# Kernel optimization log

Measured on AMD Instinct MI355X. Metric: run time of the kernel, lower is better.

The kernel has to match this reference:

```python
import jax, jax.numpy as jnp
import numpy as np

N_NODES = 2708      # hardcoded in GCN.__init__ (DictLearn(2708, nfeat/2))
NFEAT = 4096
M_DICT = NFEAT // 2 # dictionary atoms
NHID = 1024
NCLASS = 64
POWER_ITER = 100
FISTA_ITER = 20


def power_method(W, key):
    # nm -> largest eigenvalue of W^T W (sigma_max(W)^2)
    X0 = jax.random.normal(key, (1, W.shape[1]), dtype=W.dtype)
    def body(i, carry):
        X, _ = carry
        Xn = (X @ W.T) @ W
        nm = jnp.linalg.norm(Xn)
        return (Xn / nm, nm)
    _, nm = jax.lax.fori_loop(0, POWER_ITER, body, (X0, jnp.float32(1.0)))
    return nm


def soft_threshold(X, lam):
    return jnp.sign(X) * jax.nn.relu(jnp.abs(X) - lam)


def fista(Y, W, lam, key):
    # torch sets W.requires_grad_(False) during sparse coding
    Ws = jax.lax.stop_gradient(W)
    c = power_method(Ws, key)
    eta = 1.0 / c
    Gamma0 = soft_threshold((eta * Ws).T @ Y, lam)   # (m, nfeat)
    Ynorm = jnp.linalg.norm(Y)
    def step(carry, _):
        Gamma, Z, t = carry
        residual = Ws @ Z - Y                         # (n, nfeat)
        Gamma_new = soft_threshold(Z - eta * (Ws.T @ residual), lam / c)
        t_new = (1.0 + jnp.sqrt(1.0 + 4.0 * t * t)) / 2.0
        Z_new = Gamma_new + (t - 1.0) / t_new * (Gamma_new - Gamma)
        nrm = jnp.linalg.norm(residual) / Ynorm
        return (Gamma_new, Z_new, t_new), nrm
    (Gamma, _, _), norms = jax.lax.scan(
        step, (Gamma0, Gamma0, jnp.float32(1.0)), None, length=FISTA_ITER)
    return Gamma, norms


def setup_inputs() -> dict:
    key = jax.random.key(0)
    ks = jax.random.split(key, 7)
    x = jax.random.normal(ks[0], (N_NODES, NFEAT), dtype=jnp.float32)
    # dense stand-in for the normalized sparse adjacency; scaled to keep activations sane
    adj = jax.random.uniform(ks[1], (N_NODES, N_NODES), dtype=jnp.float32) / N_NODES
    stdv1 = 1.0 / np.sqrt(NHID)
    gc1_w = jax.random.uniform(ks[2], (NFEAT, NHID), minval=-stdv1, maxval=stdv1, dtype=jnp.float32)
    gc1_b = jax.random.uniform(ks[3], (NHID,), minval=-stdv1, maxval=stdv1, dtype=jnp.float32)
    stdv2 = 1.0 / np.sqrt(NCLASS)
    gc2_w = jax.random.uniform(ks[4], (NHID, NCLASS), minval=-stdv2, maxval=stdv2, dtype=jnp.float32)
    gc2_b = jax.random.uniform(ks[5], (NCLASS,), minval=-stdv2, maxval=stdv2, dtype=jnp.float32)
    # torch normalizes W in-place via .data, so the learnable leaf IS the normalized dict
    W_dict = jax.random.normal(ks[6], (N_NODES, M_DICT), dtype=jnp.float32)
    W_dict = W_dict / jnp.linalg.norm(W_dict, axis=0, keepdims=True)
    return {"x": x, "adj": adj, "gc1_w": gc1_w, "gc1_b": gc1_b,
            "gc2_w": gc2_w, "gc2_b": gc2_b, "W_dict": W_dict, "K": 1}


def reference(x, adj, gc1_w, gc1_b, gc2_w, gc2_b, W_dict, K):
    # SC='fista' (the only dimensionally consistent path); K acts as lamda
    lam = jnp.float32(K)
    Gamma, norms = fista(x, W_dict, lam, jax.random.key(1))  # (m, nfeat)
    x_dec = W_dict @ Gamma                                   # (n, nfeat)
    h = jax.nn.relu(adj @ (x_dec @ gc1_w) + gc1_b)           # dropout is identity in eval
    out = adj @ (h @ gc2_w) + gc2_b
    return jax.nn.log_softmax(out, axis=1), x_dec, Gamma, norms
```

## Files before the change

### kernel.cpp

```cpp
#include <hip/hip_runtime.h>
#include <cstdint>
#include <cmath>

#define NN_ 2708
#define NF_ 4096
#define MD_ 2048
#define NH_ 1024
#define NC_ 64
#define FITER 20
#define KPAD 2720


typedef _Float16 half8_t __attribute__((ext_vector_type(8)));
typedef _Float16 half4_t __attribute__((ext_vector_type(4)));
typedef float floatx4_t __attribute__((ext_vector_type(4)));

__device__ __forceinline__ float softt(float v, float t) {
    float a = fabsf(v) - t;
    a = a > 0.f ? a : 0.f;
    return copysignf(a, v);
}

__device__ __forceinline__ float blockReduceSum(float v, float* red) {
    int lane = threadIdx.x & 63, wid = threadIdx.x >> 6;
    #pragma unroll
    for (int off = 32; off; off >>= 1) v += __shfl_down(v, off);
    if (lane == 0) red[wid] = v;
    __syncthreads();
    if (wid == 0) {
        int nw = (blockDim.x + 63) >> 6;
        float r = (lane < nw) ? red[lane] : 0.f;
        #pragma unroll
        for (int off = 4; off; off >>= 1) r += __shfl_down(r, off);
        if (lane == 0) red[0] = r;
    }
    __syncthreads();
    float out = red[0];
    __syncthreads();
    return out;
}

__device__ __forceinline__ float erfinv_f(float x) {
    float w = -log1pf(-x * x);
    float p;
    if (w < 5.0f) {
        w -= 2.5f;
        p = 2.81022636e-08f;
        p = fmaf(p, w, 3.43273939e-07f);
        p = fmaf(p, w, -3.5233877e-06f);
        p = fmaf(p, w, -4.39150654e-06f);
        p = fmaf(p, w, 0.00021858087f);
        p = fmaf(p, w, -0.00125372503f);
        p = fmaf(p, w, -0.00417768164f);
        p = fmaf(p, w, 0.246640727f);
        p = fmaf(p, w, 1.50140941f);
    } else {
        w = sqrtf(w) - 3.0f;
        p = -0.000200214257f;
        p = fmaf(p, w, 0.000100950558f);
        p = fmaf(p, w, 0.00134934322f);
        p = fmaf(p, w, -0.00367342844f);
        p = fmaf(p, w, 0.00573950773f);
        p = fmaf(p, w, -0.0076224613f);
        p = fmaf(p, w, 0.00943887047f);
        p = fmaf(p, w, 1.00167406f);
        p = fmaf(p, w, 2.83297682f);
    }
    return p * x;
}

__device__ __forceinline__ float u32_to_normal(uint32_t bits) {
    uint32_t fb = (bits >> 9) | 0x3F800000u;
    float f = __uint_as_float(fb) - 1.0f;
    const float lo = -0.99999994f;
    float u = fmaf(f, 2.0f, lo);
    u = fmaxf(lo, u);
    return 1.41421356f * erfinv_f(u);
}

__global__ void init_x0_kernel(float* __restrict__ X0) {
    int i = blockIdx.x * blockDim.x + threadIdx.x;
    if (i >= MD_ / 2) return;
    uint32_t x0 = (uint32_t)i, x1 = (uint32_t)(i + MD_ / 2);
    const uint32_t k0 = 0u, k1 = 1u, k2 = 0x1BD11BDBu;
    const uint32_t ks[3] = {k0, k1, k2};
    x0 += k0; x1 += k1;
    const int rot[8] = {13, 15, 26, 6, 17, 29, 16, 24};
    #pragma unroll
    for (int g = 0; g < 5; ++g) {
        const int base = (g & 1) ? 4 : 0;
        #pragma unroll
        for (int rr = 0; rr < 4; ++rr) {
            x0 += x1;
            int r = rot[base + rr];
            x1 = (x1 << r) | (x1 >> (32 - r));
            x1 ^= x0;
        }
        x0 += ks[(g + 1) % 3];
        x1 += ks[(g + 2) % 3] + (uint32_t)(g + 1);
    }
    X0[i] = u32_to_normal(x0);
    X0[i + MD_ / 2] = u32_to_normal(x1);
}

__global__ void zero_scal_kernel(float* __restrict__ scal) {
    int t = threadIdx.x;
    if (t < 32) scal[t] = 0.f;
}

__global__ void fill0_kernel(uint32_t* __restrict__ p, int n32) {
    int i = blockIdx.x * blockDim.x + threadIdx.x;
    if (i < n32) p[i] = 0u;
}

__global__ void sumsq_kernel(const float* __restrict__ X, int n, float* __restrict__ acc) {
    __shared__ float red[8];
    float s = 0.f;
    for (size_t i = (size_t)blockIdx.x * blockDim.x + threadIdx.x; i < (size_t)n;
         i += (size_t)gridDim.x * blockDim.x) {
        float v = X[i];
        s += v * v;
    }
    s = blockReduceSum(s, red);
    if (threadIdx.x == 0) atomicAdd(acc, s);
}

__global__ void tsplit_kernel(const float* __restrict__ src, int R, int ld, int Rpad,
                              _Float16* __restrict__ hi, _Float16* __restrict__ lo) {
    __shared__ float t[32][33];
    int rb = blockIdx.y * 32, cb = blockIdx.x * 32;
    int tx = threadIdx.x & 31, ty = threadIdx.x >> 5;
    #pragma unroll
    for (int s = 0; s < 32; s += 8) {
        int r = rb + ty + s, c = cb + tx;
        t[ty + s][tx] = (r < R) ? src[(size_t)r * ld + c] : 0.f;
    }
    __syncthreads();
    #pragma unroll
    for (int s = 0; s < 32; s += 8) {
        int c = cb + ty + s, r = rb + tx;
        float v = t[tx][ty + s];
        _Float16 h = (_Float16)v;
        size_t o = (size_t)c * Rpad + r;
        hi[o] = h;
        lo[o] = (_Float16)(v - (float)h);
    }
}

__global__ void splitrows_hi_kernel(const float* __restrict__ src, int R, int C,
                                    _Float16* __restrict__ hi) {
    int r = blockIdx.x;
    _Float16* d = hi + (size_t)r * C;
    if (r < R) {
        const float* s = src + (size_t)r * C;
        for (int c = threadIdx.x * 4; c < C; c += 1024) {
            float4 v = *reinterpret_cast<const float4*>(s + c);
            half4_t h;
            h[0] = (_Float16)v.x; h[1] = (_Float16)v.y;
            h[2] = (_Float16)v.z; h[3] = (_Float16)v.w;
            *reinterpret_cast<half4_t*>(d + c) = h;
        }
    } else {
        for (int c = threadIdx.x * 4; c < C; c += 1024) {
            half4_t h = {(_Float16)0.f, (_Float16)0.f, (_Float16)0.f, (_Float16)0.f};
            *reinterpret_cast<half4_t*>(d + c) = h;
        }
    }
}

__global__ void splitadj_hi_kernel(const float* __restrict__ adj, _Float16* __restrict__ hi) {
    int r = blockIdx.x;
    bool rok = r < NN_;
    _Float16* d = hi + (size_t)r * KPAD;
    const float* s = adj + (size_t)r * NN_;
    for (int c = threadIdx.x * 4; c < KPAD; c += 1024) {
        half4_t h = {(_Float16)0.f, (_Float16)0.f, (_Float16)0.f, (_Float16)0.f};
        if (rok && c + 3 < NN_) {
            float4 v = *reinterpret_cast<const float4*>(s + c);
            h[0] = (_Float16)v.x; h[1] = (_Float16)v.y;
            h[2] = (_Float16)v.z; h[3] = (_Float16)v.w;
        }
        *reinterpret_cast<half4_t*>(d + c) = h;
    }
}

__global__ void g0_kernel(const float* __restrict__ Bm, const float* __restrict__ scal,
                          float* __restrict__ Gamma,
                          _Float16* __restrict__ Zh, _Float16* __restrict__ Zl) {
    __shared__ float t[32][33];
    int rb = blockIdx.y * 32;
    int cb = blockIdx.x * 32;
    float eta = scal[1], lam = scal[3];
    int tx = threadIdx.x & 31, ty = threadIdx.x >> 5;
    #pragma unroll
    for (int s = 0; s < 32; s += 8) {
        int r = rb + ty + s, c = cb + tx;
        float g = softt(eta * Bm[(size_t)r * NF_ + c], lam);
        Gamma[(size_t)r * NF_ + c] = g;
        t[ty + s][tx] = g;
    }
    __syncthreads();
    #pragma unroll
    for (int s = 0; s < 32; s += 8) {
        int c = cb + ty + s, r = rb + tx;
        float v = t[tx][ty + s];
        _Float16 h = (_Float16)v;
        size_t o = (size_t)c * MD_ + r;
        Zh[o] = h;
        Zl[o] = (_Float16)(v - (float)h);
    }
}

__global__ __launch_bounds__(256)
void papply_kernel(const _Float16* __restrict__ Mh, const _Float16* __restrict__ Ml,
                   const float* __restrict__ Xc, float* __restrict__ Xn, int addI) {
    __shared__ float xs[MD_];
    __shared__ float red[8];
    const int tid = threadIdx.x;
    float ss = 0.f;
    for (int k = tid; k < MD_; k += 256) { float v = Xc[k]; xs[k] = v; ss += v * v; }
    __syncthreads();
    ss = blockReduceSum(ss, red);
    float inv = 1.0f / sqrtf(ss);
    const int w = tid >> 6, l = tid & 63;
    const int r = blockIdx.x * 4 + w;
    const _Float16* mhr = Mh + (size_t)r * MD_;
    const _Float16* mlr = Ml + (size_t)r * MD_;
    float s = 0.f;
    #pragma unroll
    for (int q = 0; q < 8; ++q) {
        int o = (q * 64 + l) * 4;
        half4_t hv = *reinterpret_cast<const half4_t*>(mhr + o);
        half4_t lv = *reinterpret_cast<const half4_t*>(mlr + o);
        float4 xv = *reinterpret_cast<const float4*>(&xs[o]);
        s = fmaf((float)hv[0] + (float)lv[0], xv.x, s);
        s = fmaf((float)hv[1] + (float)lv[1], xv.y, s);
        s = fmaf((float)hv[2] + (float)lv[2], xv.z, s);
        s = fmaf((float)hv[3] + (float)lv[3], xv.w, s);
    }
    #pragma unroll
    for (int off = 32; off; off >>= 1) s += __shfl_down(s, off);
    if (l == 0) Xn[r] = (s + (addI ? xs[r] : 0.f)) * inv;
}

__global__ void pfinal_kernel(const float* __restrict__ Xf, const int* __restrict__ Kp,
                              float* __restrict__ scal) {
    __shared__ float red[8];
    float ss = 0.f;
    for (int k = threadIdx.x; k < MD_; k += 256) { float v = Xf[k]; ss += v * v; }
    ss = blockReduceSum(ss, red);
    if (threadIdx.x == 0) {
        float c = sqrtf(ss);
        float lam = (float)Kp[0];
        scal[0] = c;
        scal[1] = 1.0f / c;
        scal[2] = lam / c;
        scal[3] = lam;
    }
}

enum { ME_STORE = 0, ME_SYMSPLIT = 1, ME_SYMSPLIT_MI = 2, ME_H1 = 3, ME_SYMSPLIT16 = 4,
       ME_SPLIT_T = 5, ME_FISTAG = 6, ME_FISTAG_LAST = 7, ME_BIAS = 8, ME_BIASRELU = 9 };

__device__ __forceinline__ void stage_h(const _Float16* __restrict__ g, int row0, int K, int kk,
                                        _Float16* s, int tid) {
    const _Float16* gp = g + (size_t)(row0 + (tid >> 2)) * K + kk + ((tid & 3) << 3);
    _Float16* lp = s + ((size_t)((tid >> 6) * 64) << 3);
    __builtin_amdgcn_global_load_lds(
        (const __attribute__((address_space(1))) void*)gp,
        (__attribute__((address_space(3))) void*)lp, 16, 0, 0);
}

template <bool AFP32, bool THREE>
__global__ __launch_bounds__(512)
void mgemm_kernel(const _Float16* __restrict__ Ah, const _Float16* __restrict__ Al,
                  const float* __restrict__ Afp, int Marr,
                  const _Float16* __restrict__ Bh, const _Float16* __restrict__ Bl,
                  int K, int Mvalid, int Nvalid, int ldc,
                  float* __restrict__ C, const float* __restrict__ BmP,
                  const float* __restrict__ bias,
                  _Float16* __restrict__ Th, _Float16* __restrict__ Tl, int Tstride,
                  const float* __restrict__ scal, float betak,
                  float* __restrict__ nrm_acc, int epi) {
    constexpr bool DB = (!AFP32 && !THREE);
    constexpr int NB = DB ? 2 : 1;
    __shared__ __align__(16) _Float16 sAh[NB * 128 * 32];
    __shared__ __align__(16) _Float16 sAl[(AFP32 || THREE) ? 128 * 32 : 64];
    __shared__ __align__(16) _Float16 sBh[NB * 128 * 32];
    __shared__ __align__(16) _Float16 sBl[NB * 128 * 32];
    __shared__ float red[8];
    const int tid = threadIdx.x;
    const int w = tid >> 6, l = tid & 63;
    const int wr = w >> 2, wc = w & 3;
    const int quad = l >> 4, lc = l & 15;
    const int row0 = blockIdx.y * 128, col0 = blockIdx.x * 128;

    floatx4_t acc[4][2];
    #pragma unroll
    for (int i = 0; i < 4; ++i)
        #pragma unroll
        for (int j = 0; j < 2; ++j) {
            floatx4_t z = {0.f, 0.f, 0.f, 0.f};
            acc[i][j] = z;
        }

    if constexpr (DB) {
        stage_h(Ah, row0, K, 0, sAh, tid);
        stage_h(Bh, col0, K, 0, sBh, tid);
        stage_h(Bl, col0, K, 0, sBl, tid);
        asm volatile("s_waitcnt vmcnt(0)" ::: "memory");
        __syncthreads();
        for (int kk = 0; kk < K; kk += 32) {
            const int cur = (kk >> 5) & 1, nxt = cur ^ 1;
            if (kk + 32 < K) {
                stage_h(Ah, row0, K, kk + 32, sAh + nxt * (128 * 32), tid);
                stage_h(Bh, col0, K, kk + 32, sBh + nxt * (128 * 32), tid);
                stage_h(Bl, col0, K, kk + 32, sBl + nxt * (128 * 32), tid);
            }
            const _Float16* pA = sAh + cur * (128 * 32);
            const _Float16* pB = sBh + cur * (128 * 32);
            const _Float16* pL = sBl + cur * (128 * 32);
            half8_t fAh[4], fBh[2], fBl[2];
            #pragma unroll
            for (int i = 0; i < 4; ++i) {
                int oa = (wr * 64 + i * 16 + lc) * 32 + quad * 8;
                fAh[i] = *reinterpret_cast<const half8_t*>(&pA[oa]);
            }
            #pragma unroll
            for (int j = 0; j < 2; ++j) {
                int ob = (wc * 32 + j * 16 + lc) * 32 + quad * 8;
                fBh[j] = *reinterpret_cast<const half8_t*>(&pB[ob]);
                fBl[j] = *reinterpret_cast<const half8_t*>(&pL[ob]);
            }
            #pragma unroll
            for (int i = 0; i < 4; ++i)
                #pragma unroll
                for (int j = 0; j < 2; ++j) {
                    acc[i][j] = __builtin_amdgcn_mfma_f32_16x16x32_f16(fAh[i], fBh[j], acc[i][j], 0, 0, 0);
                    acc[i][j] = __builtin_amdgcn_mfma_f32_16x16x32_f16(fAh[i], fBl[j], acc[i][j], 0, 0, 0);
                }
            asm volatile("s_waitcnt vmcnt(0)" ::: "memory");
            __syncthreads();
        }
    } else {
        for (int kk = 0; kk < K; kk += 32) {
            if constexpr (AFP32) {
                #pragma unroll
                for (int p = 0; p < 2; ++p) {
                    int c2 = p * 512 + tid;
                    int r = c2 >> 3, k4 = (c2 & 7) << 2;
                    int gr = row0 + r;
                    gr = gr < Marr ? gr : Marr - 1;
                    float4 v = *reinterpret_cast<const float4*>(Afp + (size_t)gr * K + kk + k4);
                    half4_t hh, ll;
                    hh[0] = (_Float16)v.x; ll[0] = (_Float16)(v.x - (float)hh[0]);
                    hh[1] = (_Float16)v.y; ll[1] = (_Float16)(v.y - (float)hh[1]);
                    hh[2] = (_Float16)v.z; ll[2] = (_Float16)(v.z - (float)hh[2]);
                    hh[3] = (_Float16)v.w; ll[3] = (_Float16)(v.w - (float)hh[3]);
                    *reinterpret_cast<half4_t*>(&sAh[r * 32 + k4]) = hh;
                    *reinterpret_cast<half4_t*>(&sAl[r * 32 + k4]) = ll;
                }
            } else {
                stage_h(Ah, row0, K, kk, sAh, tid);
                if constexpr (THREE) stage_h(Al, row0, K, kk, sAl, tid);
            }
            stage_h(Bh, col0, K, kk, sBh, tid);
            stage_h(Bl, col0, K, kk, sBl, tid);
            asm volatile("s_waitcnt vmcnt(0)" ::: "memory");
            __syncthreads();

            half8_t fAh[4], fAl[4], fBh[2], fBl[2];
            #pragma unroll
            for (int i = 0; i < 4; ++i) {
                int oa = (wr * 64 + i * 16 + lc) * 32 + quad * 8;
                fAh[i] = *reinterpret_cast<const half8_t*>(&sAh[oa]);
                if constexpr (THREE) fAl[i] = *reinterpret_cast<const half8_t*>(&sAl[oa]);
            }
            #pragma unroll
            for (int j = 0; j < 2; ++j) {
                int ob = (wc * 32 + j * 16 + lc) * 32 + quad * 8;
                fBh[j] = *reinterpret_cast<const half8_t*>(&sBh[ob]);
                fBl[j] = *reinterpret_cast<const half8_t*>(&sBl[ob]);
            }
            #pragma unroll
            for (int i = 0; i < 4; ++i)
                #pragma unroll
                for (int j = 0; j < 2; ++j) {
                    acc[i][j] = __builtin_amdgcn_mfma_f32_16x16x32_f16(fAh[i], fBh[j], acc[i][j], 0, 0, 0);
                    acc[i][j] = __builtin_amdgcn_mfma_f32_16x16x32_f16(fAh[i], fBl[j], acc[i][j], 0, 0, 0);
                    if constexpr (THREE)
                        acc[i][j] = __builtin_amdgcn_mfma_f32_16x16x32_f16(fAl[i], fBh[j], acc[i][j], 0, 0, 0);
                }
            __syncthreads();
        }
    }

    float eta = 0.f, thr = 0.f;
    if (epi == ME_FISTAG || epi == ME_FISTAG_LAST) { eta = scal[1]; thr = scal[2]; }
    float rsq = 0.f;
    #pragma unroll
    for (int i = 0; i < 4; ++i) {
        int grow0 = row0 + wr * 64 + i * 16 + quad * 4;
        bool rowok = grow0 < Mvalid;
        #pragma unroll
        for (int j = 0; j < 2; ++j) {
            int gcol = col0 + wc * 32 + j * 16 + lc;
            bool colok = gcol < Nvalid;
            floatx4_t v = acc[i][j];
            if (epi == ME_STORE) {
                if (rowok && colok) {
                    #pragma unroll
                    for (int r = 0; r < 4; ++r) C[(size_t)(grow0 + r) * ldc + gcol] = v[r];
                }
            } else if (epi == ME_SYMSPLIT || epi == ME_SYMSPLIT_MI || epi == ME_H1 ||
                       epi == ME_SYMSPLIT16) {
                #pragma unroll
                for (int r = 0; r < 4; ++r) {
                    float vv = v[r];
                    float dg = ((grow0 + r) == gcol) ? 1.f : 0.f;
                    size_t o = (size_t)(grow0 + r) * Tstride + gcol;
                    if (epi == ME_SYMSPLIT_MI) {
                        vv -= dg;
                    } else if (epi == ME_H1) {
                        float ev = (float)Ah[o] + (float)Al[o];
                        vv = (vv + 2.f * ev + dg) * 0.0625f;
                    } else if (epi == ME_SYMSPLIT16) {
                        vv *= 16.f;
                    }
                    _Float16 h = (_Float16)vv;
                    Th[o] = h;
                    Tl[o] = (_Float16)(vv - (float)h);
                }
            } else if (epi == ME_SPLIT_T) {
                if (rowok && colok) {
                    half4_t hh, ll;
                    #pragma unroll
                    for (int r = 0; r < 4; ++r) {
                        _Float16 h = (_Float16)v[r];
                        hh[r] = h; ll[r] = (_Float16)(v[r] - (float)h);
                    }
                    size_t to = (size_t)gcol * Tstride + grow0;
                    *reinterpret_cast<half4_t*>(&Th[to]) = hh;
                    *reinterpret_cast<half4_t*>(&Tl[to]) = ll;
                }
            } else if (epi == ME_FISTAG || epi == ME_FISTAG_LAST) {
                size_t to = (size_t)gcol * Tstride + grow0;
                half4_t zh = *reinterpret_cast<const half4_t*>(&Bh[to]);
                half4_t zl = *reinterpret_cast<const half4_t*>(&Bl[to]);
                half4_t oh, ol;
                #pragma unroll
                for (int r = 0; r < 4; ++r) {
                    float z = (float)zh[r] + (float)zl[r];
                    float p = v[r] + z;
                    float bi = BmP[(size_t)(grow0 + r) * NF_ + gcol];
                    rsq = fmaf(z, p - 2.0f * bi, rsq);
                    float g = z - eta * (p - bi);
                    float gn = softt(g, thr);
                    size_t ci = (size_t)(grow0 + r) * NF_ + gcol;
                    float gold = C[ci];
                    C[ci] = gn;
                    float zo = (epi == ME_FISTAG) ? (gn + betak * (gn - gold)) : gn;
                    _Float16 h = (_Float16)zo;
                    oh[r] = h; ol[r] = (_Float16)(zo - (float)h);
                }
                *reinterpret_cast<half4_t*>(&Th[to]) = oh;
                *reinterpret_cast<half4_t*>(&Tl[to]) = ol;
            } else {
                if (rowok && colok) {
                    #pragma unroll
                    for (int r = 0; r < 4; ++r) {
                        float s = v[r] + bias[gcol];
                        if (epi == ME_BIASRELU) s = s > 0.f ? s : 0.f;
                        C[(size_t)(grow0 + r) * ldc + gcol] = s;
                    }
                }
            }
        }
    }
    if (epi == ME_FISTAG || epi == ME_FISTAG_LAST) {
        float tot = blockReduceSum(rsq, red);
        if (tid == 0) atomicAdd(nrm_acc, tot);
    }
}

__global__ void logsoftmax_kernel(const float* __restrict__ O, float* __restrict__ out) {
    int row = blockIdx.x * 4 + (threadIdx.x >> 6);
    int lane = threadIdx.x & 63;
    if (row >= NN_) return;
    float v = O[row * NC_ + lane];
    float m = v;
    #pragma unroll
    for (int off = 32; off; off >>= 1) m = fmaxf(m, __shfl_xor(m, off));
    float e = expf(v - m);
    float s = e;
    #pragma unroll
    for (int off = 32; off; off >>= 1) s += __shfl_xor(s, off);
    out[row * NC_ + lane] = (v - m) - logf(s);
}

__global__ void norms_kernel(const float* __restrict__ scal, float* __restrict__ nout) {
    int k = threadIdx.x;
    if (k < FITER) {
        float ysq = scal[4];
        float v = scal[5 + k] + ysq;
        nout[k] = sqrtf(fmaxf(v, 0.f)) / sqrtf(ysq);
    }
}

static inline void launch_m(bool afp32, bool three, dim3 grid,
                            const _Float16* Ah, const _Float16* Al,
                            const float* Afp, int Marr,
                            const _Float16* Bh, const _Float16* Bl,
                            int K, int Mvalid, int Nvalid, int ldc,
                            float* C, const float* BmP, const float* bias,
                            _Float16* Th, _Float16* Tl, int Tstride,
                            const float* scal, float betak, float* nrm, int epi,
                            hipStream_t s) {
    if (afp32)
        mgemm_kernel<true, true><<<grid, dim3(512), 0, s>>>(
            Ah, Al, Afp, Marr, Bh, Bl, K, Mvalid, Nvalid, ldc, C, BmP, bias,
            Th, Tl, Tstride, scal, betak, nrm, epi);
    else if (three)
        mgemm_kernel<false, true><<<grid, dim3(512), 0, s>>>(
            Ah, Al, Afp, Marr, Bh, Bl, K, Mvalid, Nvalid, ldc, C, BmP, bias,
            Th, Tl, Tstride, scal, betak, nrm, epi);
    else
        mgemm_kernel<false, false><<<grid, dim3(512), 0, s>>>(
            Ah, Al, Afp, Marr, Bh, Bl, K, Mvalid, Nvalid, ldc, C, BmP, bias,
            Th, Tl, Tstride, scal, betak, nrm, epi);
}

extern "C" void kernel_launch(void* const* d_in, const int* in_sizes, int n_in,
                              void* d_out, int out_size, void* d_ws, size_t ws_size,
                              hipStream_t stream) {
    const float* x     = (const float*)d_in[0];
    const float* adj   = (const float*)d_in[1];
    const float* gc1_w = (const float*)d_in[2];
    const float* gc1_b = (const float*)d_in[3];
    const float* gc2_w = (const float*)d_in[4];
    const float* gc2_b = (const float*)d_in[5];
    const float* Wd    = (const float*)d_in[6];
    const int*   Kp    = (const int*)d_in[7];

    float* out = (float*)d_out;
    float* logp    = out;
    float* x_dec   = logp + (size_t)NN_ * NC_;
    float* Gamma   = x_dec + (size_t)NN_ * NF_;
    float* norms_o = Gamma + (size_t)MD_ * NF_;

    char* wsb = (char*)d_ws;
    const size_t OFF_R1 = 16512;
    const size_t OFF_R2 = OFF_R1 + 16777216;
    const size_t OFF_R3 = OFF_R2 + 33554432;
    const size_t OFF_R4 = OFF_R3 + 33554432;
    float* scal = (float*)wsb;
    float* Xa   = scal + 32;
    float* Xb   = Xa + MD_;
    _Float16* Eh = (_Float16*)(wsb + OFF_R1);
    _Float16* El = Eh + (size_t)MD_ * MD_;
    float* Bm = (float*)(wsb + OFF_R2);
    _Float16* Wt_hi  = (_Float16*)(wsb + OFF_R3);
    _Float16* Wt_lo  = Wt_hi + (size_t)MD_ * KPAD;
    _Float16* xth_hi = Wt_lo + (size_t)MD_ * KPAD;
    _Float16* xth_lo = (_Float16*)(wsb + OFF_R4);
    _Float16* HA_hi = (_Float16*)(wsb + OFF_R4);
    _Float16* HA_lo = HA_hi + (size_t)MD_ * MD_;
    _Float16* HB_hi = (_Float16*)(wsb + OFF_R3);
    _Float16* HB_lo = HB_hi + (size_t)MD_ * MD_;
    _Float16* ZA_hi = (_Float16*)(wsb + OFF_R3);
    _Float16* ZA_lo = ZA_hi + (size_t)NF_ * MD_;
    _Float16* ZB_hi = (_Float16*)x_dec;
    _Float16* ZB_lo = ZB_hi + (size_t)NF_ * MD_;
    _Float16* adjT_hi = (_Float16*)(wsb + OFF_R2);
    _Float16* xwT_hi  = (_Float16*)(wsb + OFF_R2 + 15319040);
    _Float16* xwT_lo  = xwT_hi + (size_t)NH_ * KPAD;
    _Float16* g1t_hi  = (_Float16*)(wsb + OFF_R1);
    _Float16* g1t_lo  = g1t_hi + (size_t)NH_ * NF_;
    _Float16* xdh     = (_Float16*)(wsb + OFF_R3);
    float*    hbuf    = (float*)(wsb + OFF_R3);
    _Float16* Wh      = (_Float16*)(wsb + OFF_R4);
    _Float16* g2t_hi  = (_Float16*)(wsb + OFF_R4 + 11534336);
    _Float16* g2t_lo  = g2t_hi + (size_t)128 * NH_;
    _Float16* hwT_hi  = (_Float16*)(wsb + OFF_R4 + 12058624);
    _Float16* hwT_lo  = hwT_hi + (size_t)128 * KPAD;
    float*    obuf    = (float*)(wsb + OFF_R4 + 13451264);

    const _Float16* nullh = nullptr;
    float* nullf = nullptr;

    zero_scal_kernel<<<1, 64, 0, stream>>>(scal);
    init_x0_kernel<<<4, 256, 0, stream>>>(Xa);
    sumsq_kernel<<<1024, 256, 0, stream>>>(x, NN_ * NF_, scal + 4);

    tsplit_kernel<<<dim3(MD_ / 32, KPAD / 32), 256, 0, stream>>>(Wd, NN_, MD_, KPAD, Wt_hi, Wt_lo);
    launch_m(false, true, dim3(16, 16), Wt_hi, Wt_lo, nullptr, 0, Wt_hi, Wt_lo,
             KPAD, MD_, MD_, 0, nullf, nullptr, nullptr, Eh, El, MD_,
             scal, 0.f, nullptr, ME_SYMSPLIT_MI, stream);
    for (int half = 0; half < 2; ++half) {
        tsplit_kernel<<<dim3(MD_ / 32, KPAD / 32), 256, 0, stream>>>(
            x + half * 2048, NN_, NF_, KPAD, xth_hi, xth_lo);
        launch_m(false, false, dim3(16, 16), Wt_hi, Wt_lo, nullptr, 0, xth_hi, xth_lo,
                 KPAD, MD_, MD_, NF_, Bm + half * 2048, nullptr, nullptr,
                 nullptr, nullptr, 0, scal, 0.f, nullptr, ME_STORE, stream);
    }
    launch_m(false, false, dim3(16, 16), Eh, El, nullptr, 0, Eh, El,
             MD_, MD_, MD_, 0, nullf, nullptr, nullptr, HA_hi, HA_lo, MD_,
             scal, 0.f, nullptr, ME_H1, stream);
    launch_m(false, false, dim3(16, 16), HA_hi, HA_lo, nullptr, 0, HA_hi, HA_lo,
             MD_, MD_, MD_, 0, nullf, nullptr, nullptr, HB_hi, HB_lo, MD_,
             scal, 0.f, nullptr, ME_SYMSPLIT, stream);
    launch_m(false, false, dim3(16, 16), HB_hi, HB_lo, nullptr, 0, HB_hi, HB_lo,
             MD_, MD_, MD_, 0, nullf, nullptr, nullptr, HA_hi, HA_lo, MD_,
             scal, 0.f, nullptr, ME_SYMSPLIT, stream);
    launch_m(false, false, dim3(16, 16), HA_hi, HA_lo, nullptr, 0, HA_hi, HA_lo,
             MD_, MD_, MD_, 0, nullf, nullptr, nullptr, HB_hi, HB_lo, MD_,
             scal, 0.f, nullptr, ME_SYMSPLIT, stream);
    launch_m(false, false, dim3(16, 16), HB_hi, HB_lo, nullptr, 0, HB_hi, HB_lo,
             MD_, MD_, MD_, 0, nullf, nullptr, nullptr, HA_hi, HA_lo, MD_,
             scal, 0.f, nullptr, ME_SYMSPLIT16, stream);
    for (int it = 0; it < 7; ++it) {
        const _Float16* mh = (it < 3) ? HA_hi : Eh;
        const _Float16* ml = (it < 3) ? HA_lo : El;
        const float* xin = (it & 1) ? Xb : Xa;
        float* xout = (it & 1) ? Xa : Xb;
        papply_kernel<<<MD_ / 4, 256, 0, stream>>>(mh, ml, xin, xout, (it >= 3) ? 1 : 0);
    }
    pfinal_kernel<<<1, 256, 0, stream>>>(Xb, Kp, scal);
    g0_kernel<<<dim3(NF_ / 32, MD_ / 32), 256, 0, stream>>>(Bm, scal, Gamma, ZA_hi, ZA_lo);

    {
        float t = 1.f;
        for (int k = 0; k < FITER; ++k) {
            float tn = (1.0f + sqrtf(1.0f + (4.0f * t) * t)) / 2.0f;
            float beta = (t - 1.0f) / tn;
            t = tn;
            _Float16* in_hi  = (k & 1) ? ZB_hi : ZA_hi;
            _Float16* in_lo  = (k & 1) ? ZB_lo : ZA_lo;
            _Float16* out_hi = (k & 1) ? ZA_hi : ZB_hi;
            _Float16* out_lo = (k & 1) ? ZA_lo : ZB_lo;
            launch_m(false, false, dim3(32, 16), Eh, El, nullptr, 0, in_hi, in_lo,
                     MD_, MD_, NF_, NF_, Gamma, Bm, nullptr,
                     out_hi, out_lo, MD_, scal, beta, scal + 5 + k,
                     (k == FITER - 1) ? ME_FISTAG_LAST : ME_FISTAG, stream);
        }
    }

    splitadj_hi_kernel<<<2816, 256, 0, stream>>>(adj, adjT_hi);
    splitrows_hi_kernel<<<2816, 256, 0, stream>>>(Wd, NN_, MD_, Wh);
    launch_m(false, false, dim3(32, 22), Wh, Wh, nullptr, 0, ZA_hi, ZA_lo,
             MD_, NN_, NF_, NF_, x_dec, nullptr, nullptr,
             nullptr, nullptr, 0, scal, 0.f, nullptr, ME_STORE, stream);
    splitrows_hi_kernel<<<2816, 256, 0, stream>>>(x_dec, NN_, NF_, xdh);
    tsplit_kernel<<<dim3(NH_ / 32, NF_ / 32), 256, 0, stream>>>(gc1_w, NF_, NH_, NF_, g1t_hi, g1t_lo);
    fill0_kernel<<<(2785280 + 255) / 256, 256, 0, stream>>>((uint32_t*)xwT_hi, 2785280);
    launch_m(false, false, dim3(8, 22), xdh, xdh, nullptr, 0, g1t_hi, g1t_lo,
             NF_, NN_, NH_, 0, nullf, nullptr, nullptr,
             xwT_hi, xwT_lo, KPAD, scal, 0.f, nullptr, ME_SPLIT_T, stream);
    launch_m(false, false, dim3(8, 22), adjT_hi, adjT_hi, nullptr, 0, xwT_hi, xwT_lo,
             KPAD, NN_, NH_, NH_, hbuf, nullptr, gc1_b,
             nullptr, nullptr, 0, scal, 0.f, nullptr, ME_BIASRELU, stream);
    fill0_kernel<<<(131072 + 255) / 256, 256, 0, stream>>>((uint32_t*)g2t_hi, 131072);
    tsplit_kernel<<<dim3(NC_ / 32, NH_ / 32), 256, 0, stream>>>(gc2_w, NH_, NC_, NH_, g2t_hi, g2t_lo);
    fill0_kernel<<<(348160 + 255) / 256, 256, 0, stream>>>((uint32_t*)hwT_hi, 348160);
    launch_m(true, true, dim3(1, 22), nullh, nullh, hbuf, NN_, g2t_hi, g2t_lo,
             NH_, NN_, NC_, 0, nullf, nullptr, nullptr,
             hwT_hi, hwT_lo, KPAD, scal, 0.f, nullptr, ME_SPLIT_T, stream);
    launch_m(false, false, dim3(1, 22), adjT_hi, adjT_hi, nullptr, 0, hwT_hi, hwT_lo,
             KPAD, NN_, NC_, NC_, obuf, nullptr, gc2_b,
             nullptr, nullptr, 0, scal, 0.f, nullptr, ME_BIAS, stream);
    logsoftmax_kernel<<<(NN_ + 3) / 4, 256, 0, stream>>>(obuf, logp);
    norms_kernel<<<1, 32, 0, stream>>>(scal, norms_o);
}
```

Baseline: 3.352 ms.

## Swizzle LDS tiles to avoid bank conflicts and double-buffer the three-product GEMM path

Applies an XOR swizzle to the 8-half chunk index within each 32-wide LDS row, in both the global_load_lds staging and the fragment reads, so MFMA operand loads from shared memory spread across banks. It also extends the double-buffered prefetch pipeline to the THREE (split A low part) variant, which was previously single-buffered. Shared memory is merged into one array sized per template variant, and the reduction scratch now aliases the tile buffers. This trades higher LDS use (possibly lower occupancy for THREE) for fewer bank conflicts and overlap of loads with MFMA work.

```diff
diff --git a/kernel.cpp b/kernel.cpp
--- a/kernel.cpp
+++ b/kernel.cpp
@@ -264,7 +264,9 @@
 
 __device__ __forceinline__ void stage_h(const _Float16* __restrict__ g, int row0, int K, int kk,
                                         _Float16* s, int tid) {
-    const _Float16* gp = g + (size_t)(row0 + (tid >> 2)) * K + kk + ((tid & 3) << 3);
+    const int row = tid >> 2;
+    const int kg = (tid & 3) ^ ((row >> 1) & 3);
+    const _Float16* gp = g + (size_t)(row0 + row) * K + kk + (kg << 3);
     _Float16* lp = s + ((size_t)((tid >> 6) * 64) << 3);
     __builtin_amdgcn_global_load_lds(
         (const __attribute__((address_space(1))) void*)gp,
@@ -282,18 +284,16 @@
                   _Float16* __restrict__ Th, _Float16* __restrict__ Tl, int Tstride,
                   const float* __restrict__ scal, float betak,
                   float* __restrict__ nrm_acc, int epi) {
-    constexpr bool DB = (!AFP32 && !THREE);
-    constexpr int NB = DB ? 2 : 1;
-    __shared__ __align__(16) _Float16 sAh[NB * 128 * 32];
-    __shared__ __align__(16) _Float16 sAl[(AFP32 || THREE) ? 128 * 32 : 64];
-    __shared__ __align__(16) _Float16 sBh[NB * 128 * 32];
-    __shared__ __align__(16) _Float16 sBl[NB * 128 * 32];
-    __shared__ float red[8];
+    constexpr int TILE = 128 * 32;
+    constexpr int NT = AFP32 ? 4 : (THREE ? 8 : 6);
+    __shared__ __align__(16) _Float16 smem[NT * TILE];
+    float* red = (float*)smem;
     const int tid = threadIdx.x;
     const int w = tid >> 6, l = tid & 63;
     const int wr = w >> 2, wc = w & 3;
     const int quad = l >> 4, lc = l & 15;
     const int row0 = blockIdx.y * 128, col0 = blockIdx.x * 128;
+    const int qs = (quad ^ ((lc >> 1) & 3)) << 3;
 
     floatx4_t acc[4][2];
     #pragma unroll
@@ -304,33 +304,41 @@
             acc[i][j] = z;
         }
 
-    if constexpr (DB) {
-        stage_h(Ah, row0, K, 0, sAh, tid);
-        stage_h(Bh, col0, K, 0, sBh, tid);
-        stage_h(Bl, col0, K, 0, sBl, tid);
+    if constexpr (!AFP32) {
+        _Float16* bAh = smem;
+        _Float16* bAl = smem + 2 * TILE;
+        _Float16* bBh = smem + (THREE ? 4 : 2) * TILE;
+        _Float16* bBl = smem + (THREE ? 6 : 4) * TILE;
+        stage_h(Ah, row0, K, 0, bAh, tid);
+        if constexpr (THREE) stage_h(Al, row0, K, 0, bAl, tid);
+        stage_h(Bh, col0, K, 0, bBh, tid);
+        stage_h(Bl, col0, K, 0, bBl, tid);
         asm volatile("s_waitcnt vmcnt(0)" ::: "memory");
         __syncthreads();
         for (int kk = 0; kk < K; kk += 32) {
             const int cur = (kk >> 5) & 1, nxt = cur ^ 1;
             if (kk + 32 < K) {
-                stage_h(Ah, row0, K, kk + 32, sAh + nxt * (128 * 32), tid);
-                stage_h(Bh, col0, K, kk + 32, sBh + nxt * (128 * 32), tid);
-                stage_h(Bl, col0, K, kk + 32, sBl + nxt * (128 * 32), tid);
+                stage_h(Ah, row0, K, kk + 32, bAh + nxt * TILE, tid);
+                if constexpr (THREE) stage_h(Al, row0, K, kk + 32, bAl + nxt * TILE, tid);
+                stage_h(Bh, col0, K, kk + 32, bBh + nxt * TILE, tid);
+                stage_h(Bl, col0, K, kk + 32, bBl + nxt * TILE, tid);
             }
-            const _Float16* pA = sAh + cur * (128 * 32);
-            const _Float16* pB = sBh + cur * (128 * 32);
-            const _Float16* pL = sBl + cur * (128 * 32);
-            half8_t fAh[4], fBh[2], fBl[2];
+            const _Float16* pAh = bAh + cur * TILE;
+            const _Float16* pAl = bAl + cur * TILE;
+            const _Float16* pBh = bBh + cur * TILE;
+            const _Float16* pBl = bBl + cur * TILE;
+            half8_t fAh[4], fAl[4], fBh[2], fBl[2];
             #pragma unroll
             for (int i = 0; i < 4; ++i) {
-                int oa = (wr * 64 + i * 16 + lc) * 32 + quad * 8;
-                fAh[i] = *reinterpret_cast<const half8_t*>(&pA[oa]);
+                int oa = (wr * 64 + i * 16 + lc) * 32 + qs;
+                fAh[i] = *reinterpret_cast<const half8_t*>(&pAh[oa]);
+                if constexpr (THREE) fAl[i] = *reinterpret_cast<const half8_t*>(&pAl[oa]);
             }
             #pragma unroll
             for (int j = 0; j < 2; ++j) {
-                int ob = (wc * 32 + j * 16 + lc) * 32 + quad * 8;
-                fBh[j] = *reinterpret_cast<const half8_t*>(&pB[ob]);
-                fBl[j] = *reinterpret_cast<const half8_t*>(&pL[ob]);
+                int ob = (wc * 32 + j * 16 + lc) * 32 + qs;
+                fBh[j] = *reinterpret_cast<const half8_t*>(&pBh[ob]);
+                fBl[j] = *reinterpret_cast<const half8_t*>(&pBl[ob]);
             }
             #pragma unroll
             for (int i = 0; i < 4; ++i)
@@ -338,31 +346,33 @@
                 for (int j = 0; j < 2; ++j) {
                     acc[i][j] = __builtin_amdgcn_mfma_f32_16x16x32_f16(fAh[i], fBh[j], acc[i][j], 0, 0, 0);
                     acc[i][j] = __builtin_amdgcn_mfma_f32_16x16x32_f16(fAh[i], fBl[j], acc[i][j], 0, 0, 0);
+                    if constexpr (THREE)
+                        acc[i][j] = __builtin_amdgcn_mfma_f32_16x16x32_f16(fAl[i], fBh[j], acc[i][j], 0, 0, 0);
                 }
             asm volatile("s_waitcnt vmcnt(0)" ::: "memory");
             __syncthreads();
         }
     } else {
+        _Float16* sAh = smem;
+        _Float16* sAl = smem + TILE;
+        _Float16* sBh = smem + 2 * TILE;
+        _Float16* sBl = smem + 3 * TILE;
         for (int kk = 0; kk < K; kk += 32) {
-            if constexpr (AFP32) {
-                #pragma unroll
-                for (int p = 0; p < 2; ++p) {
-                    int c2 = p * 512 + tid;
-                    int r = c2 >> 3, k4 = (c2 & 7) << 2;
-                    int gr = row0 + r;
-                    gr = gr < Marr ? gr : Marr - 1;
-                    float4 v = *reinterpret_cast<const float4*>(Afp + (size_t)gr * K + kk + k4);
-                    half4_t hh, ll;
-                    hh[0] = (_Float16)v.x; ll[0] = (_Float16)(v.x - (float)hh[0]);
-                    hh[1] = (_Float16)v.y; ll[1] = (_Float16)(v.y - (float)hh[1]);
-                    hh[2] = (_Float16)v.z; ll[2] = (_Float16)(v.z - (float)hh[2]);
-                    hh[3] = (_Float16)v.w; ll[3] = (_Float16)(v.w - (float)hh[3]);
-                    *reinterpret_cast<half4_t*>(&sAh[r * 32 + k4]) = hh;
-                    *reinterpret_cast<half4_t*>(&sAl[r * 32 + k4]) = ll;
-                }
-            } else {
-                stage_h(Ah, row0, K, kk, sAh, tid);
-                if constexpr (THREE) stage_h(Al, row0, K, kk, sAl, tid);
+            #pragma unroll
+            for (int p = 0; p < 2; ++p) {
+                int c2 = p * 512 + tid;
+                int r = c2 >> 3, k4 = (c2 & 7) << 2;
+                int gr = row0 + r;
+                gr = gr < Marr ? gr : Marr - 1;
+                float4 v = *reinterpret_cast<const float4*>(Afp + (size_t)gr * K + kk + k4);
+                half4_t hh, ll;
+                hh[0] = (_Float16)v.x; ll[0] = (_Float16)(v.x - (float)hh[0]);
+                hh[1] = (_Float16)v.y; ll[1] = (_Float16)(v.y - (float)hh[1]);
+                hh[2] = (_Float16)v.z; ll[2] = (_Float16)(v.z - (float)hh[2]);
+                hh[3] = (_Float16)v.w; ll[3] = (_Float16)(v.w - (float)hh[3]);
+                int sw = (((k4 >> 3) ^ ((r >> 1) & 3)) << 3) | (k4 & 7);
+                *reinterpret_cast<half4_t*>(&sAh[r * 32 + sw]) = hh;
+                *reinterpret_cast<half4_t*>(&sAl[r * 32 + sw]) = ll;
             }
             stage_h(Bh, col0, K, kk, sBh, tid);
             stage_h(Bl, col0, K, kk, sBl, tid);
@@ -372,13 +382,13 @@
             half8_t fAh[4], fAl[4], fBh[2], fBl[2];
             #pragma unroll
             for (int i = 0; i < 4; ++i) {
-                int oa = (wr * 64 + i * 16 + lc) * 32 + quad * 8;
+                int oa = (wr * 64 + i * 16 + lc) * 32 + qs;
                 fAh[i] = *reinterpret_cast<const half8_t*>(&sAh[oa]);
-                if constexpr (THREE) fAl[i] = *reinterpret_cast<const half8_t*>(&sAl[oa]);
+                fAl[i] = *reinterpret_cast<const half8_t*>(&sAl[oa]);
             }
             #pragma unroll
             for (int j = 0; j < 2; ++j) {
-                int ob = (wc * 32 + j * 16 + lc) * 32 + quad * 8;
+                int ob = (wc * 32 + j * 16 + lc) * 32 + qs;
                 fBh[j] = *reinterpret_cast<const half8_t*>(&sBh[ob]);
                 fBl[j] = *reinterpret_cast<const half8_t*>(&sBl[ob]);
             }
@@ -388,8 +398,7 @@
                 for (int j = 0; j < 2; ++j) {
                     acc[i][j] = __builtin_amdgcn_mfma_f32_16x16x32_f16(fAh[i], fBh[j], acc[i][j], 0, 0, 0);
                     acc[i][j] = __builtin_amdgcn_mfma_f32_16x16x32_f16(fAh[i], fBl[j], acc[i][j], 0, 0, 0);
-                    if constexpr (THREE)
-                        acc[i][j] = __builtin_amdgcn_mfma_f32_16x16x32_f16(fAl[i], fBh[j], acc[i][j], 0, 0, 0);
+                    acc[i][j] = __builtin_amdgcn_mfma_f32_16x16x32_f16(fAl[i], fBh[j], acc[i][j], 0, 0, 0);
                 }
             __syncthreads();
         }
```

Measured after the change: 3.145 ms. 6.2% less time.
